# Performance work log

Measured on AMD Instinct MI355X. Metric: run time of the kernel, lower is better.

The kernel has to match this reference:

```python
import jax, jax.numpy as jnp
import numpy as np

G = 20000          # num_genes
B = 256            # batch_size
NNZ = 640000       # sparse adjacency nonzeros (avg degree 32)
K = 2              # PPR iterations
ALPHA = 0.1
NUM_CLASS = 33


def _spmm(rows, cols, vals, x):
    # y = A @ x with A sparse COO [G, G], x dense [G, B]
    return jax.ops.segment_sum(vals[:, None] * x[cols], rows, num_segments=G)


def setup_inputs() -> dict:
    key = jax.random.key(0)
    ks = jax.random.split(key, 18)
    inp = {
        "x_sample": jax.random.normal(ks[0], (B * G,), jnp.float32),
        "x_TF": jax.random.normal(ks[1], (B * G,), jnp.float32),
        "adj_rows": jax.random.randint(ks[2], (NNZ,), 0, G, jnp.int32),
        "adj_cols": jax.random.randint(ks[3], (NNZ,), 0, G, jnp.int32),
        "adj_vals": jax.random.uniform(ks[4], (NNZ,), jnp.float32) / 32.0,
        "adjT_rows": jax.random.randint(ks[5], (NNZ,), 0, G, jnp.int32),
        "adjT_cols": jax.random.randint(ks[6], (NNZ,), 0, G, jnp.int32),
        "adjT_vals": jax.random.uniform(ks[7], (NNZ,), jnp.float32) / 32.0,
        # learned scalar affine params (torch.rand(1))
        "emb_mut": jax.random.uniform(ks[8], (1,), jnp.float32),
        "bias_mut": jax.random.uniform(ks[9], (1,), jnp.float32),
        "emb_exp": jax.random.uniform(ks[10], (1,), jnp.float32),
        "bias_exp": jax.random.uniform(ks[11], (1,), jnp.float32),
        # MLP params (torch Linear layout: W [out, in])
        "W1": jax.random.normal(ks[12], (1024, G), jnp.float32) * (1.0 / np.sqrt(G)),
        "b1": jnp.zeros((1024,), jnp.float32),
        "W2": jax.random.normal(ks[13], (128, 1024), jnp.float32) * (1.0 / 32.0),
        "b2": jnp.zeros((128,), jnp.float32),
        "W3": jax.random.normal(ks[14], (NUM_CLASS, 128), jnp.float32) * (1.0 / np.sqrt(128.0)),
        "b3": jnp.zeros((NUM_CLASS,), jnp.float32),
    }
    return inp


def reference(x_sample, x_TF, adj_rows, adj_cols, adj_vals,
              adjT_rows, adjT_cols, adjT_vals,
              emb_mut, bias_mut, emb_exp, bias_exp,
              W1, b1, W2, b2, W3, b3):
    # scalar affine embedding + relu
    emb_m = jax.nn.relu(emb_mut * x_sample + bias_mut)   # [B*G]
    emb_e = jax.nn.relu(emb_exp * x_TF + bias_exp)       # [B*G]
    xs = emb_m.reshape(B, G).T                            # [G, B]
    xt = emb_e.reshape(B, G).T                            # [G, B]
    hs, ht = xs, xt
    one_m_a = 1.0 - ALPHA
    for _ in range(K):
        xs = _spmm(adj_rows, adj_cols, adj_vals, one_m_a * xs)
        xt = _spmm(adjT_rows, adjT_cols, adjT_vals, one_m_a * xt)
    xs = xs + ALPHA * hs
    xt = xt + ALPHA * ht
    hadamard = (xs * xt).T                                # [B, G]
    h1 = jax.nn.relu(hadamard @ W1.T + b1)                # [B, 1024]
    h2 = jax.nn.relu(h1 @ W2.T + b2)                      # [B, 128]
    return h2 @ W3.T + b3                                 # [B, num_class]
```

## Files before the change

kernel.cpp:

```cpp
#include <hip/hip_runtime.h>
#include <hip/hip_fp16.h>

#define G_   20000
#define B_   256
#define NNZ_ 640000
#define KCH_ 640
#define NZ_  32
#define NBUK 157
#define BCAP 4608
#define EPB  4000

typedef float f4 __attribute__((ext_vector_type(4)));
typedef _Float16 h8 __attribute__((ext_vector_type(8)));

__global__ __launch_bounds__(256) void zero_kernel(unsigned int* p, int n) {
    int i = blockIdx.x * 256 + threadIdx.x;
    if (i < n) p[i] = 0u;
}

__global__ __launch_bounds__(256) void embed_kernel(
        const float* __restrict__ xsamp, const float* __restrict__ xtf,
        const float* __restrict__ em, const float* __restrict__ bm,
        const float* __restrict__ ee, const float* __restrict__ be,
        __half* __restrict__ X0s, __half* __restrict__ X0t) {
    __shared__ float lds[64][65];
    const int t  = threadIdx.x;
    const int gb = blockIdx.x * 64, bb = blockIdx.y * 64;
    const float a_m = em[0], c_m = bm[0], a_e = ee[0], c_e = be[0];
    const int gl = t & 63, brow0 = t >> 6;
    const int cl = t & 31, row0  = t >> 5;
    const int g_l = gb + gl;
#pragma unroll
    for (int r = 0; r < 16; r++) {
        int bl = brow0 + r * 4;
        float v = 0.f;
        if (g_l < G_) v = xsamp[(size_t)(bb + bl) * G_ + g_l];
        lds[bl][gl] = fmaxf(a_m * v + c_m, 0.f);
    }
    __syncthreads();
#pragma unroll
    for (int r = 0; r < 8; r++) {
        int gl2 = row0 + r * 8;
        int g = gb + gl2;
        if (g < G_) {
            __half2 hv = __floats2half2_rn(lds[cl * 2][gl2], lds[cl * 2 + 1][gl2]);
            *(__half2*)(X0s + (size_t)g * B_ + bb + cl * 2) = hv;
        }
    }
    __syncthreads();
#pragma unroll
    for (int r = 0; r < 16; r++) {
        int bl = brow0 + r * 4;
        float v = 0.f;
        if (g_l < G_) v = xtf[(size_t)(bb + bl) * G_ + g_l];
        lds[bl][gl] = fmaxf(a_e * v + c_e, 0.f);
    }
    __syncthreads();
#pragma unroll
    for (int r = 0; r < 8; r++) {
        int gl2 = row0 + r * 8;
        int g = gb + gl2;
        if (g < G_) {
            __half2 hv = __floats2half2_rn(lds[cl * 2][gl2], lds[cl * 2 + 1][gl2]);
            *(__half2*)(X0t + (size_t)g * B_ + bb + cl * 2) = hv;
        }
    }
}

__global__ __launch_bounds__(256) void binsort_kernel(
        const int* __restrict__ rA, const int* __restrict__ cA, const float* __restrict__ vA,
        const int* __restrict__ rB, const int* __restrict__ cB, const float* __restrict__ vB,
        int2* __restrict__ metaA, int* __restrict__ cntA,
        int2* __restrict__ metaB, int* __restrict__ cntB) {
    __shared__ int2 stage[EPB];
    __shared__ unsigned char bkid[EPB];
    __shared__ int hist[NBUK], lstart[NBUK], gbase[NBUK];
    const int t = threadIdx.x;
    const int base = blockIdx.x * EPB;
    const int* rows; const int* colsp; const float* valsp; int2* meta; int* cnt;
    if (blockIdx.y == 0) { rows = rA; colsp = cA; valsp = vA; meta = metaA; cnt = cntA; }
    else                 { rows = rB; colsp = cB; valsp = vB; meta = metaB; cnt = cntB; }

    for (int i = t; i < NBUK; i += 256) hist[i] = 0;
    __syncthreads();
    for (int i = t; i < EPB; i += 256)
        atomicAdd(&hist[rows[base + i] >> 7], 1);
    __syncthreads();
    if (t == 0) {
        int s = 0;
        for (int b = 0; b < NBUK; b++) { lstart[b] = s; s += hist[b]; }
    }
    __syncthreads();
    if (t < NBUK) hist[t] = lstart[t];
    __syncthreads();
    for (int i = t; i < EPB; i += 256) {
        int r = rows[base + i];
        int c = colsp[base + i];
        float v = valsp[base + i];
        int b = r >> 7;
        int p = atomicAdd(&hist[b], 1);
        stage[p] = make_int2(((r & 127) << 24) | (c * (B_ * 2)),
                             __float_as_int(0.9f * v));
        bkid[p] = (unsigned char)b;
    }
    __syncthreads();
    if (t < NBUK) gbase[t] = atomicAdd(&cnt[t], hist[t] - lstart[t]);
    __syncthreads();
    for (int i = t; i < EPB; i += 256) {
        int b = bkid[i];
        meta[(size_t)b * BCAP + gbase[b] + (i - lstart[b])] = stage[i];
    }
}

__global__ __launch_bounds__(256) void rowsort_kernel(
        const int2* __restrict__ metaA, const int* __restrict__ cntA,
        int2* __restrict__ sortedA, int* __restrict__ rpA,
        const int2* __restrict__ metaB, const int* __restrict__ cntB,
        int2* __restrict__ sortedB, int* __restrict__ rpB) {
    __shared__ int2 stage[BCAP];
    __shared__ int2 sorted[BCAP];
    __shared__ int hist[2048];
    __shared__ int scanbuf[256];
    __shared__ int rowstart[128];
    __shared__ int carr[NBUK];
    const int t = threadIdx.x;
    const int buk = blockIdx.x;
    const int2* meta; const int* cnt; int2* outp; int* rp;
    if (blockIdx.y == 0) { meta = metaA; cnt = cntA; outp = sortedA; rp = rpA; }
    else                 { meta = metaB; cnt = cntB; outp = sortedB; rp = rpB; }

    if (t < NBUK) carr[t] = cnt[t];
    for (int i = t; i < 2048; i += 256) hist[i] = 0;
    __syncthreads();
    int bukStart = 0;
    const int nE = carr[buk];
    for (int b = 0; b < buk; b++) bukStart += carr[b];

    const int2* mp = meta + (size_t)buk * BCAP;
    for (int i = t; i < nE; i += 256) {
        int2 m = mp[i];
        stage[i] = m;
        unsigned ux = (unsigned)m.x;
        int key = ((ux >> 24) << 4) | ((ux & 0xFFFFFF) >> 20);
        atomicAdd(&hist[key], 1);
    }
    __syncthreads();
    int loc[8];
    {
        int s = 0;
#pragma unroll
        for (int i = 0; i < 8; i++) { loc[i] = s; s += hist[t * 8 + i]; }
        scanbuf[t] = s;
    }
    __syncthreads();
    for (int off = 1; off < 256; off <<= 1) {
        int v = scanbuf[t];
        int add = (t >= off) ? scanbuf[t - off] : 0;
        __syncthreads();
        scanbuf[t] = v + add;
        __syncthreads();
    }
    {
        int pre = (t == 0) ? 0 : scanbuf[t - 1];
#pragma unroll
        for (int i = 0; i < 8; i++) hist[t * 8 + i] = pre + loc[i];
    }
    __syncthreads();
    if (t < 128) rowstart[t] = hist[t << 4];
    __syncthreads();
    for (int i = t; i < nE; i += 256) {
        int2 m = stage[i];
        unsigned ux = (unsigned)m.x;
        int key = ((ux >> 24) << 4) | ((ux & 0xFFFFFF) >> 20);
        int p = atomicAdd(&hist[key], 1);
        sorted[p] = make_int2(m.x & 0xFFFFFF, m.y);
    }
    __syncthreads();
    for (int i = t; i < nE; i += 256)
        outp[bukStart + i] = sorted[i];
    if (t < 128) {
        int g = buk * 128 + t;
        if (g < G_) rp[g] = bukStart + rowstart[t];
    }
    if (buk == NBUK - 1 && t == 0) rp[G_] = bukStart + nE;
}

__global__ __launch_bounds__(256) void spmm_kernel(
        const int* __restrict__ rpA, const int2* __restrict__ metaA,
        const __half* __restrict__ xinA, __half* __restrict__ xoutA,
        const int* __restrict__ rpB, const int2* __restrict__ metaB,
        const __half* __restrict__ xinB, __half* __restrict__ xoutB) {
    const int bid   = blockIdx.x;
    const int combo = bid & 1;
    const int t = threadIdx.x;
    const int wave = t >> 6, lane = t & 63;
    const int g = (bid >> 1) * 4 + wave;
    const int* rp; const int2* meta; const __half* xin; __half* xout;
    if (combo == 0) { rp = rpA; meta = metaA; xin = xinA; xout = xoutA; }
    else            { rp = rpB; meta = metaB; xin = xinB; xout = xoutB; }
    const int beg = __builtin_amdgcn_readfirstlane(rp[g]);
    const int n   = __builtin_amdgcn_readfirstlane(rp[g + 1]) - beg;
    const char* xb = (const char*)xin + lane * 8;
    float a0 = 0.f, a1 = 0.f, a2 = 0.f, a3 = 0.f;
    int e = 0;
    for (; e + 8 <= n; e += 8) {
        int2 m[8];
        uint2 r[8];
#pragma unroll
        for (int j = 0; j < 8; j++) m[j] = meta[beg + e + j];
#pragma unroll
        for (int j = 0; j < 8; j++) r[j] = *(const uint2*)(xb + m[j].x);
#pragma unroll
        for (int j = 0; j < 8; j++) {
            float v = __int_as_float(m[j].y);
            float2 l = __half22float2(*(__half2*)&r[j].x);
            float2 h = __half22float2(*(__half2*)&r[j].y);
            a0 = fmaf(v, l.x, a0); a1 = fmaf(v, l.y, a1);
            a2 = fmaf(v, h.x, a2); a3 = fmaf(v, h.y, a3);
        }
    }
    if (e + 4 <= n) {
        int2 m[4];
        uint2 r[4];
#pragma unroll
        for (int j = 0; j < 4; j++) m[j] = meta[beg + e + j];
#pragma unroll
        for (int j = 0; j < 4; j++) r[j] = *(const uint2*)(xb + m[j].x);
#pragma unroll
        for (int j = 0; j < 4; j++) {
            float v = __int_as_float(m[j].y);
            float2 l = __half22float2(*(__half2*)&r[j].x);
            float2 h = __half22float2(*(__half2*)&r[j].y);
            a0 = fmaf(v, l.x, a0); a1 = fmaf(v, l.y, a1);
            a2 = fmaf(v, h.x, a2); a3 = fmaf(v, h.y, a3);
        }
        e += 4;
    }
    for (; e < n; ++e) {
        int2 m = meta[beg + e];
        float v = __int_as_float(m.y);
        uint2 r = *(const uint2*)(xb + m.x);
        float2 l = __half22float2(*(__half2*)&r.x), h = __half22float2(*(__half2*)&r.y);
        a0 = fmaf(v, l.x, a0); a1 = fmaf(v, l.y, a1);
        a2 = fmaf(v, h.x, a2); a3 = fmaf(v, h.y, a3);
    }
    __half2 o0 = __floats2half2_rn(a0, a1);
    __half2 o1 = __floats2half2_rn(a2, a3);
    uint2 ov;
    ov.x = *(unsigned*)&o0;
    ov.y = *(unsigned*)&o1;
    *(uint2*)((char*)xout + (size_t)g * (B_ * 2) + lane * 8) = ov;
}

__global__ __launch_bounds__(256) void combine_kernel(
        const __half* __restrict__ X2s, const __half* __restrict__ X0s,
        const __half* __restrict__ X2t, const __half* __restrict__ X0t,
        __half* __restrict__ hadBK) {
    __shared__ float lds[64][65];
    const int t = threadIdx.x;
    const int gb = blockIdx.x * 64, bb = blockIdx.y * 64;
    const int cl = t & 31, row0 = t >> 5;
#pragma unroll
    for (int r = 0; r < 8; r++) {
        int gl = row0 + r * 8;
        int g = gb + gl;
        float px = 0.f, py = 0.f;
        if (g < G_) {
            size_t idx = (size_t)g * B_ + bb + cl * 2;
            float2 x2s = __half22float2(*(const __half2*)(X2s + idx));
            float2 x0s = __half22float2(*(const __half2*)(X0s + idx));
            float2 x2t = __half22float2(*(const __half2*)(X2t + idx));
            float2 x0t = __half22float2(*(const __half2*)(X0t + idx));
            px = (x2s.x + 0.1f * x0s.x) * (x2t.x + 0.1f * x0t.x);
            py = (x2s.y + 0.1f * x0s.y) * (x2t.y + 0.1f * x0t.y);
        }
        lds[gl][cl * 2]     = px;
        lds[gl][cl * 2 + 1] = py;
    }
    __syncthreads();
#pragma unroll
    for (int r = 0; r < 8; r++) {
        int bl = row0 + r * 8;
        int g0 = gb + cl * 2;
        if (g0 < G_) {
            __half2 hv = __floats2half2_rn(lds[cl * 2][bl], lds[cl * 2 + 1][bl]);
            *(__half2*)(hadBK + (size_t)(bb + bl) * G_ + g0) = hv;
        }
    }
}

__global__ __launch_bounds__(512) void gemm1_kernel(
        const __half* __restrict__ hadBK, const float* __restrict__ W1,
        float* __restrict__ part) {
    __shared__ _Float16 a_lds[2][256][40];
    __shared__ _Float16 b_lds[2][128][40];
    const int t = threadIdx.x;
    const int lane = t & 63, wid = t >> 6;
    const int wm = wid >> 1, wn = wid & 1;
    const int l15 = lane & 15, l4 = lane >> 4;
    const int ob = blockIdx.x * 128;
    const int kb = blockIdx.y * KCH_;
    int kend = kb + KCH_; if (kend > G_) kend = G_;
    const int nsteps = (kend - kb) >> 5;
    const int ar = t >> 1, ah = t & 1;
    const int br = t >> 2, bs = t & 3;
    const _Float16* hadH = (const _Float16*)hadBK;
    const _Float16* asrc = hadH + (size_t)ar * G_ + ah * 16;
    const float*    bsrc = W1 + (size_t)(ob + br) * G_ + bs * 8;
    f4 acc[4][4] = {};
    h8 ra0 = *(const h8*)(asrc + kb);
    h8 ra1 = *(const h8*)(asrc + kb + 8);
    f4 rb0 = *(const f4*)(bsrc + kb);
    f4 rb1 = *(const f4*)(bsrc + kb + 4);
    *(h8*)&a_lds[0][ar][ah * 16]     = ra0;
    *(h8*)&a_lds[0][ar][ah * 16 + 8] = ra1;
    {
        h8 h;
        h[0] = (_Float16)rb0[0]; h[1] = (_Float16)rb0[1];
        h[2] = (_Float16)rb0[2]; h[3] = (_Float16)rb0[3];
        h[4] = (_Float16)rb1[0]; h[5] = (_Float16)rb1[1];
        h[6] = (_Float16)rb1[2]; h[7] = (_Float16)rb1[3];
        *(h8*)&b_lds[0][br][bs * 8] = h;
    }
    __syncthreads();
    int p = 0;
    for (int s = 0; s < nsteps; ++s) {
        if (s + 1 < nsteps) {
            const int k1 = kb + (s + 1) * 32;
            ra0 = *(const h8*)(asrc + k1);
            ra1 = *(const h8*)(asrc + k1 + 8);
            rb0 = *(const f4*)(bsrc + k1);
            rb1 = *(const f4*)(bsrc + k1 + 4);
        }
        h8 af[4], bf[4];
#pragma unroll
        for (int m = 0; m < 4; m++)
            af[m] = *(const h8*)&a_lds[p][wm * 64 + m * 16 + l15][l4 * 8];
#pragma unroll
        for (int n = 0; n < 4; n++)
            bf[n] = *(const h8*)&b_lds[p][wn * 64 + n * 16 + l15][l4 * 8];
#pragma unroll
        for (int m = 0; m < 4; m++)
#pragma unroll
            for (int n = 0; n < 4; n++)
                acc[m][n] = __builtin_amdgcn_mfma_f32_16x16x32_f16(
                    af[m], bf[n], acc[m][n], 0, 0, 0);
        if (s + 1 < nsteps) {
            *(h8*)&a_lds[p ^ 1][ar][ah * 16]     = ra0;
            *(h8*)&a_lds[p ^ 1][ar][ah * 16 + 8] = ra1;
            h8 h;
            h[0] = (_Float16)rb0[0]; h[1] = (_Float16)rb0[1];
            h[2] = (_Float16)rb0[2]; h[3] = (_Float16)rb0[3];
            h[4] = (_Float16)rb1[0]; h[5] = (_Float16)rb1[1];
            h[6] = (_Float16)rb1[2]; h[7] = (_Float16)rb1[3];
            *(h8*)&b_lds[p ^ 1][br][bs * 8] = h;
            __syncthreads();
            p ^= 1;
        }
    }
    const size_t zoff = (size_t)blockIdx.y * (B_ * 1024);
#pragma unroll
    for (int m = 0; m < 4; m++)
#pragma unroll
        for (int n = 0; n < 4; n++)
#pragma unroll
            for (int j = 0; j < 4; j++) {
                int b = wm * 64 + m * 16 + l4 * 4 + j;
                int o = ob + wn * 64 + n * 16 + l15;
                part[zoff + (size_t)b * 1024 + o] = acc[m][n][j];
            }
}

__global__ __launch_bounds__(128) void gemm23_kernel(
        const float* __restrict__ part, const float* __restrict__ b1,
        const float* __restrict__ W2, const float* __restrict__ b2,
        const float* __restrict__ W3, const float* __restrict__ b3,
        float* __restrict__ out) {
    __shared__ float h1row[1024];
    __shared__ float h2[128];
    const int b = blockIdx.x, t = threadIdx.x;
#pragma unroll
    for (int seg = 0; seg < 2; seg++) {
        int o4 = t + seg * 128;
        f4 s = {0.f, 0.f, 0.f, 0.f};
        for (int z = 0; z < NZ_; z++)
            s += ((const f4*)(part + (size_t)z * 262144 + (size_t)b * 1024))[o4];
        s += ((const f4*)b1)[o4];
        f4 r;
        r[0] = fmaxf(s[0], 0.f); r[1] = fmaxf(s[1], 0.f);
        r[2] = fmaxf(s[2], 0.f); r[3] = fmaxf(s[3], 0.f);
        ((f4*)h1row)[o4] = r;
    }
    __syncthreads();
    {
        float acc = b2[t];
        const f4* w  = (const f4*)(W2 + (size_t)t * 1024);
        const f4* hr = (const f4*)h1row;
        for (int k = 0; k < 256; k++) {
            f4 wv = w[k], hv = hr[k];
            acc += wv[0] * hv[0] + wv[1] * hv[1] + wv[2] * hv[2] + wv[3] * hv[3];
        }
        h2[t] = fmaxf(acc, 0.f);
    }
    __syncthreads();
    if (t < 33) {
        float acc = b3[t];
        const f4* w  = (const f4*)(W3 + (size_t)t * 128);
        const f4* hv = (const f4*)h2;
#pragma unroll
        for (int k = 0; k < 32; k++) {
            f4 a = w[k], x = hv[k];
            acc += a[0] * x[0] + a[1] * x[1] + a[2] * x[2] + a[3] * x[3];
        }
        out[b * 33 + t] = acc;
    }
}

extern "C" void kernel_launch(void* const* d_in, const int* in_sizes, int n_in,
                              void* d_out, int out_size, void* d_ws, size_t ws_size,
                              hipStream_t stream) {
    const float* x_sample  = (const float*)d_in[0];
    const float* x_TF      = (const float*)d_in[1];
    const int*   adj_rows  = (const int*)d_in[2];
    const int*   adj_cols  = (const int*)d_in[3];
    const float* adj_vals  = (const float*)d_in[4];
    const int*   adjT_rows = (const int*)d_in[5];
    const int*   adjT_cols = (const int*)d_in[6];
    const float* adjT_vals = (const float*)d_in[7];
    const float* emb_mut   = (const float*)d_in[8];
    const float* bias_mut  = (const float*)d_in[9];
    const float* emb_exp   = (const float*)d_in[10];
    const float* bias_exp  = (const float*)d_in[11];
    const float* W1 = (const float*)d_in[12];
    const float* b1 = (const float*)d_in[13];
    const float* W2 = (const float*)d_in[14];
    const float* b2 = (const float*)d_in[15];
    const float* W3 = (const float*)d_in[16];
    const float* b3 = (const float*)d_in[17];
    float* out = (float*)d_out;

    char* w = (char*)d_ws;
    auto alloc = [&](size_t bytes) {
        char* p = w; w += (bytes + 255) & ~(size_t)255; return p;
    };
    __half* X0s = (__half*)alloc(5120000 * 2);
    __half* X1s = (__half*)alloc(5120000 * 2);
    __half* X2s = (__half*)alloc(5120000 * 2);
    __half* X0t = (__half*)alloc(5120000 * 2);
    __half* X1t = (__half*)alloc(5120000 * 2);
    __half* X2t = (__half*)alloc(5120000 * 2);
    float*  part = (float*)alloc((size_t)NZ_ * 262144 * 4);
    int2*   metaA   = (int2*)alloc((size_t)NBUK * BCAP * 8);
    int2*   metaB   = (int2*)alloc((size_t)NBUK * BCAP * 8);
    int2*   sortedA = (int2*)alloc((size_t)(NNZ_ + 128) * 8);
    int2*   sortedB = (int2*)alloc((size_t)(NNZ_ + 128) * 8);
    int*    cnt   = (int*)alloc(2 * NBUK * 4);
    int*    cntA  = cnt;
    int*    cntB  = cnt + NBUK;
    int*    rpA   = (int*)alloc(20001 * 4);
    int*    rpB   = (int*)alloc(20001 * 4);
    __half* hadBK = X1s;

    zero_kernel<<<2, 256, 0, stream>>>((unsigned int*)cnt, 2 * NBUK);

    embed_kernel<<<dim3(313, 4), 256, 0, stream>>>(
        x_sample, x_TF, emb_mut, bias_mut, emb_exp, bias_exp, X0s, X0t);

    binsort_kernel<<<dim3(160, 2), 256, 0, stream>>>(
        adj_rows, adj_cols, adj_vals, adjT_rows, adjT_cols, adjT_vals,
        metaA, cntA, metaB, cntB);
    rowsort_kernel<<<dim3(NBUK, 2), 256, 0, stream>>>(
        metaA, cntA, sortedA, rpA, metaB, cntB, sortedB, rpB);

    spmm_kernel<<<10000, 256, 0, stream>>>(rpA, sortedA, X0s, X1s,
                                           rpB, sortedB, X0t, X1t);
    spmm_kernel<<<10000, 256, 0, stream>>>(rpA, sortedA, X1s, X2s,
                                           rpB, sortedB, X1t, X2t);

    combine_kernel<<<dim3(313, 4), 256, 0, stream>>>(X2s, X0s, X2t, X0t, hadBK);

    gemm1_kernel<<<dim3(8, NZ_), 512, 0, stream>>>(hadBK, W1, part);
    gemm23_kernel<<<B_, 128, 0, stream>>>(part, b1, W2, b2, W3, b3, out);
}
```

Before: 432.9 us.

## Fuse counter zeroing, simplify row sort, prefetch SpMM metadata, split gemm23 reduction

Counter zeroing moves into the first block of the embed kernel, which removes one launch. The row sort drops the column-sub-bucket key and the parallel scan and uses a 128-entry row histogram with a serial scan on one thread. The SpMM kernel now double-buffers its metadata loads across 8-edge chunks and places all A rows before all B rows instead of interleaving the two. gemm23 uses 256 threads and splits the W2 dot product into two halves, cutting the per-thread serial work. The sort no longer orders entries by column inside a row, which may lower gather locality, and the serial scan adds a short single-thread stage.

```diff
diff --git a/kernel.cpp b/kernel.cpp
--- a/kernel.cpp
+++ b/kernel.cpp
@@ -13,18 +13,16 @@
 typedef float f4 __attribute__((ext_vector_type(4)));
 typedef _Float16 h8 __attribute__((ext_vector_type(8)));
 
-__global__ __launch_bounds__(256) void zero_kernel(unsigned int* p, int n) {
-    int i = blockIdx.x * 256 + threadIdx.x;
-    if (i < n) p[i] = 0u;
-}
-
 __global__ __launch_bounds__(256) void embed_kernel(
         const float* __restrict__ xsamp, const float* __restrict__ xtf,
         const float* __restrict__ em, const float* __restrict__ bm,
         const float* __restrict__ ee, const float* __restrict__ be,
-        __half* __restrict__ X0s, __half* __restrict__ X0t) {
+        __half* __restrict__ X0s, __half* __restrict__ X0t,
+        int* __restrict__ cnt) {
     __shared__ float lds[64][65];
     const int t  = threadIdx.x;
+    if (blockIdx.x == 0 && blockIdx.y == 0)
+        for (int i = t; i < 2 * NBUK; i += 256) cnt[i] = 0;
     const int gb = blockIdx.x * 64, bb = blockIdx.y * 64;
     const float a_m = em[0], c_m = bm[0], a_e = ee[0], c_e = be[0];
     const int gl = t & 63, brow0 = t >> 6;
@@ -119,10 +117,8 @@
         int2* __restrict__ sortedB, int* __restrict__ rpB) {
     __shared__ int2 stage[BCAP];
     __shared__ int2 sorted[BCAP];
-    __shared__ int hist[2048];
-    __shared__ int scanbuf[256];
-    __shared__ int rowstart[128];
     __shared__ int carr[NBUK];
+    __shared__ int hist[128], lstart[128];
     const int t = threadIdx.x;
     const int buk = blockIdx.x;
     const int2* meta; const int* cnt; int2* outp; int* rp;
@@ -130,7 +126,7 @@
     else                 { meta = metaB; cnt = cntB; outp = sortedB; rp = rpB; }
 
     if (t < NBUK) carr[t] = cnt[t];
-    for (int i = t; i < 2048; i += 256) hist[i] = 0;
+    if (t < 128) hist[t] = 0;
     __syncthreads();
     int bukStart = 0;
     const int nE = carr[buk];
@@ -140,39 +136,20 @@
     for (int i = t; i < nE; i += 256) {
         int2 m = mp[i];
         stage[i] = m;
-        unsigned ux = (unsigned)m.x;
-        int key = ((ux >> 24) << 4) | ((ux & 0xFFFFFF) >> 20);
-        atomicAdd(&hist[key], 1);
-    }
-    __syncthreads();
-    int loc[8];
-    {
+        atomicAdd(&hist[(unsigned)m.x >> 24], 1);
+    }
+    __syncthreads();
+    if (t == 0) {
         int s = 0;
-#pragma unroll
-        for (int i = 0; i < 8; i++) { loc[i] = s; s += hist[t * 8 + i]; }
-        scanbuf[t] = s;
-    }
-    __syncthreads();
-    for (int off = 1; off < 256; off <<= 1) {
-        int v = scanbuf[t];
-        int add = (t >= off) ? scanbuf[t - off] : 0;
-        __syncthreads();
-        scanbuf[t] = v + add;
-        __syncthreads();
-    }
-    {
-        int pre = (t == 0) ? 0 : scanbuf[t - 1];
-#pragma unroll
-        for (int i = 0; i < 8; i++) hist[t * 8 + i] = pre + loc[i];
-    }
-    __syncthreads();
-    if (t < 128) rowstart[t] = hist[t << 4];
+        for (int r = 0; r < 128; r++) { lstart[r] = s; s += hist[r]; }
+    }
+    __syncthreads();
+    if (t < 128) hist[t] = lstart[t];
     __syncthreads();
     for (int i = t; i < nE; i += 256) {
         int2 m = stage[i];
-        unsigned ux = (unsigned)m.x;
-        int key = ((ux >> 24) << 4) | ((ux & 0xFFFFFF) >> 20);
-        int p = atomicAdd(&hist[key], 1);
+        int r = (unsigned)m.x >> 24;
+        int p = atomicAdd(&hist[r], 1);
         sorted[p] = make_int2(m.x & 0xFFFFFF, m.y);
     }
     __syncthreads();
@@ -180,9 +157,29 @@
         outp[bukStart + i] = sorted[i];
     if (t < 128) {
         int g = buk * 128 + t;
-        if (g < G_) rp[g] = bukStart + rowstart[t];
+        if (g < G_) rp[g] = bukStart + lstart[t];
     }
     if (buk == NBUK - 1 && t == 0) rp[G_] = bukStart + nE;
+}
+
+__device__ __forceinline__ void spmm_load8(const int2* __restrict__ mp, int base,
+                                           int2* mm) {
+#pragma unroll
+    for (int j = 0; j < 8; j++) mm[j] = mp[base + j];
+}
+__device__ __forceinline__ void spmm_proc8(const int2* mm, const char* xb,
+        float& a0, float& a1, float& a2, float& a3) {
+    uint2 r[8];
+#pragma unroll
+    for (int j = 0; j < 8; j++) r[j] = *(const uint2*)(xb + mm[j].x);
+#pragma unroll
+    for (int j = 0; j < 8; j++) {
+        float v = __int_as_float(mm[j].y);
+        float2 l = __half22float2(*(__half2*)&r[j].x);
+        float2 h = __half22float2(*(__half2*)&r[j].y);
+        a0 = fmaf(v, l.x, a0); a1 = fmaf(v, l.y, a1);
+        a2 = fmaf(v, h.x, a2); a3 = fmaf(v, h.y, a3);
+    }
 }
 
 __global__ __launch_bounds__(256) void spmm_kernel(
@@ -190,54 +187,35 @@
         const __half* __restrict__ xinA, __half* __restrict__ xoutA,
         const int* __restrict__ rpB, const int2* __restrict__ metaB,
         const __half* __restrict__ xinB, __half* __restrict__ xoutB) {
-    const int bid   = blockIdx.x;
-    const int combo = bid & 1;
+    const int bid = blockIdx.x;
+    const int isB = bid >= 5000;
+    const int idx = isB ? bid - 5000 : bid;
     const int t = threadIdx.x;
     const int wave = t >> 6, lane = t & 63;
-    const int g = (bid >> 1) * 4 + wave;
+    const int g = idx * 4 + wave;
     const int* rp; const int2* meta; const __half* xin; __half* xout;
-    if (combo == 0) { rp = rpA; meta = metaA; xin = xinA; xout = xoutA; }
-    else            { rp = rpB; meta = metaB; xin = xinB; xout = xoutB; }
+    if (!isB) { rp = rpA; meta = metaA; xin = xinA; xout = xoutA; }
+    else      { rp = rpB; meta = metaB; xin = xinB; xout = xoutB; }
     const int beg = __builtin_amdgcn_readfirstlane(rp[g]);
     const int n   = __builtin_amdgcn_readfirstlane(rp[g + 1]) - beg;
+    const int2* mp = meta + beg;
     const char* xb = (const char*)xin + lane * 8;
     float a0 = 0.f, a1 = 0.f, a2 = 0.f, a3 = 0.f;
-    int e = 0;
-    for (; e + 8 <= n; e += 8) {
-        int2 m[8];
-        uint2 r[8];
-#pragma unroll
-        for (int j = 0; j < 8; j++) m[j] = meta[beg + e + j];
-#pragma unroll
-        for (int j = 0; j < 8; j++) r[j] = *(const uint2*)(xb + m[j].x);
-#pragma unroll
-        for (int j = 0; j < 8; j++) {
-            float v = __int_as_float(m[j].y);
-            float2 l = __half22float2(*(__half2*)&r[j].x);
-            float2 h = __half22float2(*(__half2*)&r[j].y);
-            a0 = fmaf(v, l.x, a0); a1 = fmaf(v, l.y, a1);
-            a2 = fmaf(v, h.x, a2); a3 = fmaf(v, h.y, a3);
-        }
-    }
-    if (e + 4 <= n) {
-        int2 m[4];
-        uint2 r[4];
-#pragma unroll
-        for (int j = 0; j < 4; j++) m[j] = meta[beg + e + j];
-#pragma unroll
-        for (int j = 0; j < 4; j++) r[j] = *(const uint2*)(xb + m[j].x);
-#pragma unroll
-        for (int j = 0; j < 4; j++) {
-            float v = __int_as_float(m[j].y);
-            float2 l = __half22float2(*(__half2*)&r[j].x);
-            float2 h = __half22float2(*(__half2*)&r[j].y);
-            a0 = fmaf(v, l.x, a0); a1 = fmaf(v, l.y, a1);
-            a2 = fmaf(v, h.x, a2); a3 = fmaf(v, h.y, a3);
-        }
-        e += 4;
-    }
-    for (; e < n; ++e) {
-        int2 m = meta[beg + e];
+    const int nb = n >> 3;
+    int2 mA[8], mB[8];
+    if (nb > 0) spmm_load8(mp, 0, mA);
+    int b2 = 0;
+    while (b2 < nb) {
+        if (b2 + 1 < nb) spmm_load8(mp, (b2 + 1) * 8, mB);
+        spmm_proc8(mA, xb, a0, a1, a2, a3);
+        b2++;
+        if (b2 >= nb) break;
+        if (b2 + 1 < nb) spmm_load8(mp, (b2 + 1) * 8, mA);
+        spmm_proc8(mB, xb, a0, a1, a2, a3);
+        b2++;
+    }
+    for (int e = nb * 8; e < n; ++e) {
+        int2 m = mp[e];
         float v = __int_as_float(m.y);
         uint2 r = *(const uint2*)(xb + m.x);
         float2 l = __half22float2(*(__half2*)&r.x), h = __half22float2(*(__half2*)&r.y);
@@ -371,42 +349,44 @@
             }
 }
 
-__global__ __launch_bounds__(128) void gemm23_kernel(
+__global__ __launch_bounds__(256) void gemm23_kernel(
         const float* __restrict__ part, const float* __restrict__ b1,
         const float* __restrict__ W2, const float* __restrict__ b2,
         const float* __restrict__ W3, const float* __restrict__ b3,
         float* __restrict__ out) {
     __shared__ float h1row[1024];
-    __shared__ float h2[128];
+    __shared__ float h2p[2][128];
     const int b = blockIdx.x, t = threadIdx.x;
-#pragma unroll
-    for (int seg = 0; seg < 2; seg++) {
-        int o4 = t + seg * 128;
+    {
         f4 s = {0.f, 0.f, 0.f, 0.f};
+        const float* pb = part + (size_t)b * 1024;
         for (int z = 0; z < NZ_; z++)
-            s += ((const f4*)(part + (size_t)z * 262144 + (size_t)b * 1024))[o4];
-        s += ((const f4*)b1)[o4];
+            s += ((const f4*)(pb + (size_t)z * 262144))[t];
+        s += ((const f4*)b1)[t];
         f4 r;
         r[0] = fmaxf(s[0], 0.f); r[1] = fmaxf(s[1], 0.f);
         r[2] = fmaxf(s[2], 0.f); r[3] = fmaxf(s[3], 0.f);
-        ((f4*)h1row)[o4] = r;
+        ((f4*)h1row)[t] = r;
     }
     __syncthreads();
     {
-        float acc = b2[t];
-        const f4* w  = (const f4*)(W2 + (size_t)t * 1024);
-        const f4* hr = (const f4*)h1row;
-        for (int k = 0; k < 256; k++) {
+        const int o = t & 127, hh = t >> 7;
+        float acc = 0.f;
+        const f4* w  = (const f4*)(W2 + (size_t)o * 1024 + hh * 512);
+        const f4* hr = (const f4*)(h1row + hh * 512);
+        for (int k = 0; k < 128; k++) {
             f4 wv = w[k], hv = hr[k];
             acc += wv[0] * hv[0] + wv[1] * hv[1] + wv[2] * hv[2] + wv[3] * hv[3];
         }
-        h2[t] = fmaxf(acc, 0.f);
-    }
+        h2p[hh][o] = acc;
+    }
+    __syncthreads();
+    if (t < 128) h2p[0][t] = fmaxf(h2p[0][t] + h2p[1][t] + b2[t], 0.f);
     __syncthreads();
     if (t < 33) {
         float acc = b3[t];
         const f4* w  = (const f4*)(W3 + (size_t)t * 128);
-        const f4* hv = (const f4*)h2;
+        const f4* hv = (const f4*)h2p[0];
 #pragma unroll
         for (int k = 0; k < 32; k++) {
             f4 a = w[k], x = hv[k];
@@ -461,10 +441,8 @@
     int*    rpB   = (int*)alloc(20001 * 4);
     __half* hadBK = X1s;
 
-    zero_kernel<<<2, 256, 0, stream>>>((unsigned int*)cnt, 2 * NBUK);
-
     embed_kernel<<<dim3(313, 4), 256, 0, stream>>>(
-        x_sample, x_TF, emb_mut, bias_mut, emb_exp, bias_exp, X0s, X0t);
+        x_sample, x_TF, emb_mut, bias_mut, emb_exp, bias_exp, X0s, X0t, cnt);
 
     binsort_kernel<<<dim3(160, 2), 256, 0, stream>>>(
         adj_rows, adj_cols, adj_vals, adjT_rows, adjT_cols, adjT_vals,
@@ -480,5 +458,5 @@
     combine_kernel<<<dim3(313, 4), 256, 0, stream>>>(X2s, X0s, X2t, X0t, hadBK);
 
     gemm1_kernel<<<dim3(8, NZ_), 512, 0, stream>>>(hadBK, W1, part);
-    gemm23_kernel<<<B_, 128, 0, stream>>>(part, b1, W2, b2, W3, b3, out);
-}
+    gemm23_kernel<<<B_, 256, 0, stream>>>(part, b1, W2, b2, W3, b3, out);
+}
```

After: 410.0 us. 5.3% less time.
